# Kernel optimization log

Measured on AMD Instinct MI355X. Metric: run time of the kernel, lower is better.

Reference implementation:

```python
import jax, jax.numpy as jnp
import numpy as np

N = 20000   # num_perts (nodes)
E = 640000  # edges
H = 2       # attention heads
D = 64      # hidden_dim = out_dim
L = 4       # num_layers
NEG_SLOPE_ATT = 0.2    # GATv2 attention leaky_relu
NEG_SLOPE_ACT = 0.01   # F.leaky_relu default


def setup_inputs() -> dict:
    key = jax.random.key(0)
    ks = jax.random.split(key, 9)
    s = 0.1
    return {
        "edge_index": jax.random.randint(ks[0], (2, E), 0, N, dtype=jnp.int64 if jax.config.x64_enabled else jnp.int32),
        "edge_weight": jax.random.uniform(ks[1], (E,), jnp.float32),
        "pert_emb": jax.random.normal(ks[2], (N, D), jnp.float32) * s,
        "Wl": jax.random.normal(ks[3], (L, D, H * D), jnp.float32) * s,
        "bl": jnp.zeros((L, H * D), jnp.float32),
        "Wr": jax.random.normal(ks[4], (L, D, H * D), jnp.float32) * s,
        "br": jnp.zeros((L, H * D), jnp.float32),
        "att": jax.random.normal(ks[5], (L, H, D), jnp.float32) * s,
        "bias": jnp.zeros((L, D), jnp.float32),
        "Wo": jax.random.normal(ks[6], (D, D), jnp.float32) * s,
        "bo": jnp.zeros((D,), jnp.float32),
    }


def _gatv2_layer(x, src, dst, Wl, bl, Wr, br, att, bias):
    # x: [N, D] -> out: [N, D] (heads averaged, concat=False)
    xl = (x @ Wl + bl).reshape(N, H, D)  # source transform
    xr = (x @ Wr + br).reshape(N, H, D)  # target transform
    e = jax.nn.leaky_relu(xl[src] + xr[dst], NEG_SLOPE_ATT)        # [E,H,D]
    logits = jnp.einsum('ehd,hd->eh', e, att)                      # [E,H]
    # segment softmax over incoming edges per target node
    m = jax.ops.segment_max(logits, dst, num_segments=N)           # [N,H]
    m = jnp.where(jnp.isfinite(m), m, 0.0)
    ex = jnp.exp(logits - m[dst])
    denom = jax.ops.segment_sum(ex, dst, num_segments=N)           # [N,H]
    alpha = ex / (denom[dst] + 1e-16)                              # [E,H]
    msg = xl[src] * alpha[:, :, None]                              # [E,H,D]
    out = jax.ops.segment_sum(msg, dst, num_segments=N)            # [N,H,D]
    return out.mean(axis=1) + bias                                 # [N,D]


def reference(edge_index, edge_weight, pert_emb, Wl, bl, Wr, br, att, bias, Wo, bo):
    del edge_weight  # use_edge_weight=False -> edge_weight set to None
    src, dst = edge_index[0], edge_index[1]
    x = pert_emb  # embedding lookup of arange(num_perts) == full table
    for i in range(L):
        x = _gatv2_layer(x, src, dst, Wl[i], bl[i], Wr[i], br[i], att[i], bias[i])
        x = jax.nn.leaky_relu(x, NEG_SLOPE_ACT)  # dropout p=0.0 is identity
    x = x @ Wo + bo
    x = jax.nn.leaky_relu(x, NEG_SLOPE_ACT)
    return x
```

## Files before the change

### kernel.cpp

```cpp
#include <hip/hip_runtime.h>
#include <math.h>
#include <float.h>

#define NN 20000
#define EE 640000
#define HH 2
#define DD 64
#define LL 4
#define HD 128
#define CAP 80
#define GR 32
#define GEMM_BLOCKS (NN / GR)
#define SCAT_BLOCKS ((EE + 255) / 256)
#define NPB 4
#define LOG2E 1.4426950408889634f


__device__ __forceinline__ float row16_sum(float x) {
    int t;
    t = __builtin_amdgcn_update_dpp(0, __float_as_int(x), 0xB1, 0xF, 0xF, true);
    x += __int_as_float(t);
    t = __builtin_amdgcn_update_dpp(0, __float_as_int(x), 0x4E, 0xF, 0xF, true);
    x += __int_as_float(t);
    t = __builtin_amdgcn_update_dpp(0, __float_as_int(x), 0x124, 0xF, 0xF, true);
    x += __int_as_float(t);
    t = __builtin_amdgcn_update_dpp(0, __float_as_int(x), 0x128, 0xF, 0xF, true);
    x += __int_as_float(t);
    return x;
}

__device__ __forceinline__ float att_dot(float4 xv, float4 xrv, float4 atv) {
    float4 v;
    v.x = xv.x + xrv.x; v.y = xv.y + xrv.y; v.z = xv.z + xrv.z; v.w = xv.w + xrv.w;
    v.x = fmaxf(v.x, 0.f) + 0.2f * fminf(v.x, 0.f);
    v.y = fmaxf(v.y, 0.f) + 0.2f * fminf(v.y, 0.f);
    v.z = fmaxf(v.z, 0.f) + 0.2f * fminf(v.z, 0.f);
    v.w = fmaxf(v.w, 0.f) + 0.2f * fminf(v.w, 0.f);
    return fmaf(v.x, atv.x, fmaf(v.y, atv.y, fmaf(v.z, atv.z, v.w * atv.w)));
}

__global__ void __launch_bounds__(256) prep_kernel(
        const float* __restrict__ x,
        const float* __restrict__ Wl, const float* __restrict__ bl,
        const float* __restrict__ Wr, const float* __restrict__ br,
        float* __restrict__ xl, float* __restrict__ xr,
        const int* __restrict__ src, const int* __restrict__ dst,
        int* __restrict__ cnt, int* __restrict__ csr_src) {
    int tid = threadIdx.x;
    if (blockIdx.x >= GEMM_BLOCKS) {
        int e = (blockIdx.x - GEMM_BLOCKS) * 256 + tid;
        if (e < EE) {
            int d = dst[e];
            int pos = atomicAdd(&cnt[d], 1);
            if (pos < CAP) csr_src[d * CAP + pos] = src[e];
        }
        return;
    }
    __shared__ float xs[16][GR];
    __shared__ float ws[16][2 * HD];
    int row0 = blockIdx.x * GR;
    int tc = tid & 63;
    int tr = tid >> 6;
    int c0 = tc * 4;

    float4 bv;
    {
        const float* bsrc = (c0 < HD) ? (bl + c0) : (br + (c0 - HD));
        bv = *(const float4*)bsrc;
    }
    float acc[8][4];
#pragma unroll
    for (int r = 0; r < 8; ++r) {
        acc[r][0] = bv.x; acc[r][1] = bv.y; acc[r][2] = bv.z; acc[r][3] = bv.w;
    }

    int sr = tid >> 3;
    int skk = (tid & 7) * 2;

    for (int kc = 0; kc < DD; kc += 16) {
        __syncthreads();
        {
            float2 v = *(const float2*)&x[(size_t)(row0 + sr) * DD + kc + skk];
            xs[skk][sr] = v.x;
            xs[skk + 1][sr] = v.y;
        }
#pragma unroll
        for (int q = 0; q < 4; ++q) {
            int idx = tid + 256 * q;
            int kk = idx >> 6;
            int cc = (idx & 63) * 4;
            const float* srcp = (cc < HD) ? (Wl + (size_t)(kc + kk) * HD + cc)
                                          : (Wr + (size_t)(kc + kk) * HD + (cc - HD));
            *(float4*)&ws[kk][cc] = *(const float4*)srcp;
        }
        __syncthreads();
#pragma unroll
        for (int kk = 0; kk < 16; ++kk) {
            float4 wv = *(const float4*)&ws[kk][c0];
            float xv[8];
            *(float4*)&xv[0] = *(const float4*)&xs[kk][tr * 8];
            *(float4*)&xv[4] = *(const float4*)&xs[kk][tr * 8 + 4];
#pragma unroll
            for (int r = 0; r < 8; ++r) {
                acc[r][0] = fmaf(xv[r], wv.x, acc[r][0]);
                acc[r][1] = fmaf(xv[r], wv.y, acc[r][1]);
                acc[r][2] = fmaf(xv[r], wv.z, acc[r][2]);
                acc[r][3] = fmaf(xv[r], wv.w, acc[r][3]);
            }
        }
    }

    float* ybase = (c0 < HD) ? xl : xr;
    int cw = (c0 < HD) ? c0 : (c0 - HD);
#pragma unroll
    for (int r = 0; r < 8; ++r) {
        int row = row0 + tr * 8 + r;
        float4 o;
        o.x = acc[r][0]; o.y = acc[r][1]; o.z = acc[r][2]; o.w = acc[r][3];
        *(float4*)&ybase[(size_t)row * HD + cw] = o;
    }
}

template <bool FINAL>
__global__ void __launch_bounds__(256, 4) fused_aggregate(
        const float* __restrict__ xl, const float* __restrict__ xr,
        const float* __restrict__ att, const int* __restrict__ cnt,
        const int* __restrict__ csr_src, const float* __restrict__ bias,
        const float* __restrict__ Wnl, const float* __restrict__ bnl,
        const float* __restrict__ Wnr, const float* __restrict__ bnr,
        const float* __restrict__ Wo, const float* __restrict__ bo,
        float* __restrict__ xlo, float* __restrict__ xro,
        float* __restrict__ out) {
    int tid = threadIdx.x;
    int lane = tid & 63;
    int w = tid >> 6;
    int node = blockIdx.x * NPB + w;
    int g = lane >> 4;
    int fo = (lane & 15) * 4;

    __shared__ float sh_o[NPB][DD];
    __shared__ float wst[16][2 * HD];
    __shared__ int   sh_idx[NPB][CAP];

    int start = node * CAP;
    int deg = min(cnt[node], CAP);

    if (lane < CAP / 2) {
        *(int2*)&sh_idx[w][lane * 2] = *(const int2*)&csr_src[start + lane * 2];
    }

    unsigned nrow = (unsigned)node << 7;
    const float4 xra = *(const float4*)&xr[nrow + fo];
    const float4 xrb = *(const float4*)&xr[nrow + 64 + fo];
    float4 ata = *(const float4*)&att[fo];
    float4 atb = *(const float4*)&att[64 + fo];
    ata.x *= LOG2E; ata.y *= LOG2E; ata.z *= LOG2E; ata.w *= LOG2E;
    atb.x *= LOG2E; atb.y *= LOG2E; atb.z *= LOG2E; atb.w *= LOG2E;

    float sa = 0.f, sb = 0.f;
    float4 aa = {0.f, 0.f, 0.f, 0.f};
    float4 ab = {0.f, 0.f, 0.f, 0.f};

    if (deg > 0) {
        int niter = (deg + 7) >> 3;

#define IDX2(k) (*(const int2*)&sh_idx[w][8 * min((k), CAP / 8 - 1) + 2 * g])

#define GATHER(B0a, B0b, B1a, B1b, k)                                      \
        {                                                                  \
            int2 r_ = IDX2(k);                                             \
            int sl_ = 8 * (k) + 2 * g;                                     \
            int s0_ = (sl_ < deg) ? r_.x : 0;                              \
            int s1_ = (sl_ + 1 < deg) ? r_.y : 0;                          \
            unsigned q0_ = (unsigned)s0_ << 7, q1_ = (unsigned)s1_ << 7;   \
            B0a = *(const float4*)&xl[q0_ + fo];                           \
            B0b = *(const float4*)&xl[q0_ + 64 + fo];                      \
            B1a = *(const float4*)&xl[q1_ + fo];                           \
            B1b = *(const float4*)&xl[q1_ + 64 + fo];                      \
        }

#define COMPUTE(B0a, B0b, B1a, B1b, k)                                     \
        {                                                                  \
            float t0a = row16_sum(att_dot(B0a, xra, ata));                 \
            float t0b = row16_sum(att_dot(B0b, xrb, atb));                 \
            float t1a = row16_sum(att_dot(B1a, xra, ata));                 \
            float t1b = row16_sum(att_dot(B1b, xrb, atb));                 \
            int sl_ = 8 * (k) + 2 * g;                                     \
            float w0a = (sl_ < deg) ? exp2f(t0a) : 0.f;                    \
            float w1a = (sl_ + 1 < deg) ? exp2f(t1a) : 0.f;                \
            float w0b = (sl_ < deg) ? exp2f(t0b) : 0.f;                    \
            float w1b = (sl_ + 1 < deg) ? exp2f(t1b) : 0.f;                \
            sa += w0a + w1a;                                               \
            sb += w0b + w1b;                                               \
            aa.x = fmaf(w0a, B0a.x, fmaf(w1a, B1a.x, aa.x));               \
            aa.y = fmaf(w0a, B0a.y, fmaf(w1a, B1a.y, aa.y));               \
            aa.z = fmaf(w0a, B0a.z, fmaf(w1a, B1a.z, aa.z));               \
            aa.w = fmaf(w0a, B0a.w, fmaf(w1a, B1a.w, aa.w));               \
            ab.x = fmaf(w0b, B0b.x, fmaf(w1b, B1b.x, ab.x));               \
            ab.y = fmaf(w0b, B0b.y, fmaf(w1b, B1b.y, ab.y));               \
            ab.z = fmaf(w0b, B0b.z, fmaf(w1b, B1b.z, ab.z));               \
            ab.w = fmaf(w0b, B0b.w, fmaf(w1b, B1b.w, ab.w));               \
        }

        float4 A0a, A0b, A1a, A1b;
        float4 B0a, B0b, B1a, B1b;
        float4 C0a, C0b, C1a, C1b;
        float4 D0a, D0b, D1a, D1b;

        GATHER(A0a, A0b, A1a, A1b, 0);
        GATHER(B0a, B0b, B1a, B1b, 1);
        GATHER(C0a, C0b, C1a, C1b, 2);

        int it = 0;
        while (true) {
            {
                GATHER(D0a, D0b, D1a, D1b, it + 3);
                __builtin_amdgcn_sched_barrier(0);
                COMPUTE(A0a, A0b, A1a, A1b, it);
            }
            if (++it == niter) break;
            {
                GATHER(A0a, A0b, A1a, A1b, it + 3);
                __builtin_amdgcn_sched_barrier(0);
                COMPUTE(B0a, B0b, B1a, B1b, it);
            }
            if (++it == niter) break;
            {
                GATHER(B0a, B0b, B1a, B1b, it + 3);
                __builtin_amdgcn_sched_barrier(0);
                COMPUTE(C0a, C0b, C1a, C1b, it);
            }
            if (++it == niter) break;
            {
                GATHER(C0a, C0b, C1a, C1b, it + 3);
                __builtin_amdgcn_sched_barrier(0);
                COMPUTE(D0a, D0b, D1a, D1b, it);
            }
            if (++it == niter) break;
        }
#undef IDX2
#undef GATHER
#undef COMPUTE
    }

#pragma unroll
    for (int off = 16; off <= 32; off <<= 1) {
        sa += __shfl_xor(sa, off);
        aa.x += __shfl_xor(aa.x, off);
        aa.y += __shfl_xor(aa.y, off);
        aa.z += __shfl_xor(aa.z, off);
        aa.w += __shfl_xor(aa.w, off);
        sb += __shfl_xor(sb, off);
        ab.x += __shfl_xor(ab.x, off);
        ab.y += __shfl_xor(ab.y, off);
        ab.z += __shfl_xor(ab.z, off);
        ab.w += __shfl_xor(ab.w, off);
    }

    float inva = 1.0f / (sa + 1e-16f);
    float invb = 1.0f / (sb + 1e-16f);

    if (lane < 16) {
        const float4 bv = *(const float4*)&bias[fo];
        float4 o;
        o.x = fmaf(0.5f, fmaf(aa.x, inva, ab.x * invb), bv.x);
        o.y = fmaf(0.5f, fmaf(aa.y, inva, ab.y * invb), bv.y);
        o.z = fmaf(0.5f, fmaf(aa.z, inva, ab.z * invb), bv.z);
        o.w = fmaf(0.5f, fmaf(aa.w, inva, ab.w * invb), bv.w);
        o.x = o.x > 0.f ? o.x : 0.01f * o.x;
        o.y = o.y > 0.f ? o.y : 0.01f * o.y;
        o.z = o.z > 0.f ? o.z : 0.01f * o.z;
        o.w = o.w > 0.f ? o.w : 0.01f * o.w;
        *(float4*)&sh_o[w][fo] = o;
    }

    if (FINAL) {
        float* wlin = &wst[0][0];
        {
            int idx = tid * 16;
            *(float4*)&wlin[idx]      = *(const float4*)&Wo[idx];
            *(float4*)&wlin[idx + 4]  = *(const float4*)&Wo[idx + 4];
            *(float4*)&wlin[idx + 8]  = *(const float4*)&Wo[idx + 8];
            *(float4*)&wlin[idx + 12] = *(const float4*)&Wo[idx + 12];
        }
        __syncthreads();
        int j = lane;
        float acc = bo[j];
#pragma unroll 8
        for (int k = 0; k < DD; ++k) {
            acc = fmaf(sh_o[w][k], wlin[k * DD + j], acc);
        }
        acc = acc > 0.f ? acc : 0.01f * acc;
        out[(size_t)node * DD + j] = acc;
    } else {
        int c0 = lane * 4;
        float4 acc4;
        {
            const float* bsrc = (c0 < HD) ? (bnl + c0) : (bnr + (c0 - HD));
            acc4 = *(const float4*)bsrc;
        }
        for (int kc = 0; kc < DD; kc += 16) {
            __syncthreads();
#pragma unroll
            for (int q = 0; q < 4; ++q) {
                int idx = tid + 256 * q;
                int kk = idx >> 6;
                int cc = (idx & 63) * 4;
                const float* p = (cc < HD) ? (Wnl + (size_t)(kc + kk) * HD + cc)
                                           : (Wnr + (size_t)(kc + kk) * HD + (cc - HD));
                *(float4*)&wst[kk][cc] = *(const float4*)p;
            }
            __syncthreads();
#pragma unroll
            for (int kk = 0; kk < 16; ++kk) {
                float xo = sh_o[w][kc + kk];
                float4 wv = *(const float4*)&wst[kk][c0];
                acc4.x = fmaf(xo, wv.x, acc4.x);
                acc4.y = fmaf(xo, wv.y, acc4.y);
                acc4.z = fmaf(xo, wv.z, acc4.z);
                acc4.w = fmaf(xo, wv.w, acc4.w);
            }
        }
        if (c0 < HD) *(float4*)&xlo[(size_t)node * HD + c0] = acc4;
        else         *(float4*)&xro[(size_t)node * HD + (c0 - HD)] = acc4;
    }
}

extern "C" void kernel_launch(void* const* d_in, const int* in_sizes, int n_in,
                              void* d_out, int out_size, void* d_ws, size_t ws_size,
                              hipStream_t stream) {
    const int* edge_index = (const int*)d_in[0];
    const int* src = edge_index;
    const int* dst = edge_index + EE;
    const float* pert = (const float*)d_in[2];
    const float* Wl = (const float*)d_in[3];
    const float* bl = (const float*)d_in[4];
    const float* Wr = (const float*)d_in[5];
    const float* br = (const float*)d_in[6];
    const float* att = (const float*)d_in[7];
    const float* bias = (const float*)d_in[8];
    const float* Wo = (const float*)d_in[9];
    const float* bo = (const float*)d_in[10];
    float* out = (float*)d_out;

    char* w = (char*)d_ws;
    float* xlA = (float*)w;           w += (size_t)NN * HD * 4;
    float* xrA = (float*)w;           w += (size_t)NN * HD * 4;
    float* xlB = (float*)w;           w += (size_t)NN * HD * 4;
    float* xrB = (float*)w;           w += (size_t)NN * HD * 4;
    int* cnt = (int*)w;               w += (size_t)NN * 4;
    int* csr_src = (int*)w;           w += (size_t)NN * CAP * 4;

    hipMemsetAsync(cnt, 0, (size_t)NN * 4, stream);
    prep_kernel<<<GEMM_BLOCKS + SCAT_BLOCKS, 256, 0, stream>>>(
        pert, Wl, bl, Wr, br, xlA, xrA, src, dst, cnt, csr_src);

    float* xls[2] = {xlA, xlB};
    float* xrs[2] = {xrA, xrB};
    for (int l = 0; l < LL - 1; ++l) {
        fused_aggregate<false><<<NN / NPB, 256, 0, stream>>>(
            xls[l & 1], xrs[l & 1], att + (size_t)l * HD, cnt, csr_src,
            bias + (size_t)l * DD,
            Wl + (size_t)(l + 1) * DD * HD, bl + (size_t)(l + 1) * HD,
            Wr + (size_t)(l + 1) * DD * HD, br + (size_t)(l + 1) * HD,
            nullptr, nullptr,
            xls[(l + 1) & 1], xrs[(l + 1) & 1], nullptr);
    }
    fused_aggregate<true><<<NN / NPB, 256, 0, stream>>>(
        xls[(LL - 1) & 1], xrs[(LL - 1) & 1], att + (size_t)(LL - 1) * HD, cnt, csr_src,
        bias + (size_t)(LL - 1) * DD,
        nullptr, nullptr, nullptr, nullptr,
        Wo, bo, nullptr, nullptr, out);
}
```

Baseline: 315.9 us.

## Sort nodes by in-degree so aggregate blocks process similar-degree nodes

Adds a histogram kernel and a counting-sort permutation kernel that order nodes by descending (capped) in-degree. The aggregate kernel then maps each wavefront to perm[...] instead of a contiguous node index. The aim is to balance work inside each 4-wave block and to schedule heavy blocks first, reducing tail imbalance. The cost is two extra small launches, an extra indirection, and loss of contiguous node ordering for xr/output accesses.

```diff
diff --git a/kernel.cpp b/kernel.cpp
--- a/kernel.cpp
+++ b/kernel.cpp
@@ -121,11 +121,47 @@
     }
 }
 
+
+__global__ void __launch_bounds__(256) hist_kernel(const int* __restrict__ cnt,
+                                                   int* __restrict__ bins) {
+    __shared__ int lbins[CAP + 1];
+    int tid = threadIdx.x;
+    if (tid <= CAP) lbins[tid] = 0;
+    __syncthreads();
+    int i = blockIdx.x * 256 + tid;
+    if (i < NN) {
+        int d = min(cnt[i], CAP);
+        atomicAdd(&lbins[d], 1);
+    }
+    __syncthreads();
+    if (tid <= CAP && lbins[tid] > 0) atomicAdd(&bins[tid], lbins[tid]);
+}
+
+__global__ void __launch_bounds__(256) perm_kernel(const int* __restrict__ cnt,
+                                                   const int* __restrict__ bins,
+                                                   int* __restrict__ cursors,
+                                                   int* __restrict__ perm) {
+    __shared__ int start_s[CAP + 1];
+    int tid = threadIdx.x;
+    if (tid == 0) {
+        int acc = 0;
+        for (int d = CAP; d >= 0; --d) { start_s[d] = acc; acc += bins[d]; }
+    }
+    __syncthreads();
+    int i = blockIdx.x * 256 + tid;
+    if (i < NN) {
+        int d = min(cnt[i], CAP);
+        int pos = atomicAdd(&cursors[d], 1);
+        perm[start_s[d] + pos] = i;
+    }
+}
+
 template <bool FINAL>
 __global__ void __launch_bounds__(256, 4) fused_aggregate(
         const float* __restrict__ xl, const float* __restrict__ xr,
         const float* __restrict__ att, const int* __restrict__ cnt,
         const int* __restrict__ csr_src, const float* __restrict__ bias,
+        const int* __restrict__ perm,
         const float* __restrict__ Wnl, const float* __restrict__ bnl,
         const float* __restrict__ Wnr, const float* __restrict__ bnr,
         const float* __restrict__ Wo, const float* __restrict__ bo,
@@ -134,7 +170,7 @@
     int tid = threadIdx.x;
     int lane = tid & 63;
     int w = tid >> 6;
-    int node = blockIdx.x * NPB + w;
+    int node = perm[blockIdx.x * NPB + w];
     int g = lane >> 4;
     int fo = (lane & 15) * 4;
 
@@ -349,18 +385,25 @@
     float* xlB = (float*)w;           w += (size_t)NN * HD * 4;
     float* xrB = (float*)w;           w += (size_t)NN * HD * 4;
     int* cnt = (int*)w;               w += (size_t)NN * 4;
+    int* bins = (int*)w;              w += (size_t)(CAP + 1) * 4;
+    int* cursors = (int*)w;           w += (size_t)(CAP + 1) * 4;
     int* csr_src = (int*)w;           w += (size_t)NN * CAP * 4;
-
-    hipMemsetAsync(cnt, 0, (size_t)NN * 4, stream);
+    int* perm = (int*)w;              w += (size_t)NN * 4;
+
+    hipMemsetAsync(cnt, 0, (size_t)NN * 4 + 2 * (size_t)(CAP + 1) * 4, stream);
     prep_kernel<<<GEMM_BLOCKS + SCAT_BLOCKS, 256, 0, stream>>>(
         pert, Wl, bl, Wr, br, xlA, xrA, src, dst, cnt, csr_src);
+
+    int nb = (NN + 255) / 256;
+    hist_kernel<<<nb, 256, 0, stream>>>(cnt, bins);
+    perm_kernel<<<nb, 256, 0, stream>>>(cnt, bins, cursors, perm);
 
     float* xls[2] = {xlA, xlB};
     float* xrs[2] = {xrA, xrB};
     for (int l = 0; l < LL - 1; ++l) {
         fused_aggregate<false><<<NN / NPB, 256, 0, stream>>>(
             xls[l & 1], xrs[l & 1], att + (size_t)l * HD, cnt, csr_src,
-            bias + (size_t)l * DD,
+            bias + (size_t)l * DD, perm,
             Wl + (size_t)(l + 1) * DD * HD, bl + (size_t)(l + 1) * HD,
             Wr + (size_t)(l + 1) * DD * HD, br + (size_t)(l + 1) * HD,
             nullptr, nullptr,
@@ -368,7 +411,7 @@
     }
     fused_aggregate<true><<<NN / NPB, 256, 0, stream>>>(
         xls[(LL - 1) & 1], xrs[(LL - 1) & 1], att + (size_t)(LL - 1) * HD, cnt, csr_src,
-        bias + (size_t)(LL - 1) * DD,
+        bias + (size_t)(LL - 1) * DD, perm,
         nullptr, nullptr, nullptr, nullptr,
         Wo, bo, nullptr, nullptr, out);
 }
```

Result: slower. 369.0 us (+16.8%).
